# Optimization experiments

Measured on AMD Instinct MI355X. Metric: run time of the kernel, lower is better.

Reference implementation:

```python
import jax, jax.numpy as jnp
import numpy as np

D_MODEL = 1024
N_HEADS = 16
D_K = D_MODEL // N_HEADS
ROPE_BASE = 10000.0


def _rope_tables(seq_len, dim, dtype=jnp.float32):
    # standard rotary: inv_freq over even dims, angles broadcast over positions
    inv_freq = 1.0 / (ROPE_BASE ** (jnp.arange(0, dim, 2, dtype=jnp.float32) / dim))
    t = jnp.arange(seq_len, dtype=jnp.float32)
    freqs = jnp.outer(t, inv_freq)                  # [S, dim/2]
    emb = jnp.concatenate([freqs, freqs], axis=-1)   # [S, dim]
    return jnp.cos(emb).astype(dtype), jnp.sin(emb).astype(dtype)


def _rotate_half(x):
    x1, x2 = jnp.split(x, 2, axis=-1)
    return jnp.concatenate([-x2, x1], axis=-1)


def _apply_rope(x, cos, sin):
    # x: [B, H, S, d_k]; cos/sin: [S, d_k]
    return x * cos[None, None, :, :] + _rotate_half(x) * sin[None, None, :, :]


def setup_inputs() -> dict:
    key = jax.random.key(0)
    k1, k2, k3 = jax.random.split(key, 3)
    x = jax.random.normal(k1, (2, 2048, D_MODEL), dtype=jnp.float32)
    # torch Linear weights are [out, in]; store pre-transposed for x @ W
    scale = 1.0 / np.sqrt(D_MODEL)
    W_qkv = jax.random.normal(k2, (D_MODEL, 3 * D_MODEL), dtype=jnp.float32) * scale
    W_o = jax.random.normal(k3, (D_MODEL, D_MODEL), dtype=jnp.float32) * scale
    return {"x": x, "W_qkv": W_qkv, "W_o": W_o}


def reference(x, W_qkv, W_o):
    B, S, D = x.shape
    # fused QKV projection, then split into heads: [3, B, H, S, d_k]
    qkv = (x @ W_qkv).reshape(B, S, 3, N_HEADS, D_K).transpose(2, 0, 3, 1, 4)
    q, k, v = qkv[0], qkv[1], qkv[2]
    cos, sin = _rope_tables(S, D_K, x.dtype)
    q = _apply_rope(q, cos, sin)
    k = _apply_rope(k, cos, sin)
    # causal scaled dot-product attention (eval: dropout_p = 0)
    scores = jnp.einsum("bhqd,bhkd->bhqk", q, k) / jnp.sqrt(jnp.asarray(D_K, x.dtype))
    causal = jnp.tril(jnp.ones((S, S), dtype=bool))
    scores = jnp.where(causal[None, None], scores, jnp.asarray(-jnp.inf, x.dtype))
    attn = jax.nn.softmax(scores, axis=-1)
    out = jnp.einsum("bhqk,bhkd->bhqd", attn, v)          # [B, H, S, d_k]
    out = out.transpose(0, 2, 1, 3).reshape(B, S, D)       # [B, S, D]
    return out @ W_o
```

## Files before the change

### kernel.cpp

```cpp
#include <hip/hip_runtime.h>
#include <math.h>

#define B_ 2
#define S_ 2048
#define D_ 1024
#define H_ 16
#define DK_ 64
#define M_ (B_ * S_)
#define N3_ (3 * D_)

typedef __bf16 bf16;
typedef bf16 bf16x4 __attribute__((ext_vector_type(4)));
typedef bf16 bf16x8 __attribute__((ext_vector_type(8)));
typedef float f32x4 __attribute__((ext_vector_type(4)));
typedef short shortx4 __attribute__((ext_vector_type(4)));

#define GLL16(g, l)                                                     \
  __builtin_amdgcn_global_load_lds(                                     \
      (const __attribute__((address_space(1))) void*)(g),               \
      (__attribute__((address_space(3))) void*)(l), 16, 0, 0)


__global__ __launch_bounds__(256) void prep_k(
    const float* __restrict__ x, const float* __restrict__ Wqkv,
    const float* __restrict__ Wo, bf16* __restrict__ xb,
    bf16* __restrict__ Wqkv_bt, bf16* __restrict__ Wo_bt) {
  const int bx = blockIdx.x;
  if (bx < 4096) {
    int i = bx * 256 + threadIdx.x;
    float4 v = ((const float4*)x)[i];
    bf16x4 o = {(bf16)v.x, (bf16)v.y, (bf16)v.z, (bf16)v.w};
    ((bf16x4*)xb)[i] = o;
    return;
  }
  __shared__ float t[32][33];
  const float* src;
  bf16* dst;
  int R, C, cx, cy;
  if (bx < 4096 + 3072) {
    int b2 = bx - 4096;
    src = Wqkv; dst = Wqkv_bt; R = D_; C = N3_;
    cx = b2 % 96; cy = b2 / 96;
  } else {
    int b2 = bx - 7168;
    src = Wo; dst = Wo_bt; R = D_; C = D_;
    cx = b2 & 31; cy = b2 >> 5;
  }
  int r0 = cy * 32, c0 = cx * 32;
  int tx = threadIdx.x & 31, ty = threadIdx.x >> 5;
#pragma unroll
  for (int rr = 0; rr < 32; rr += 8)
    t[ty + rr][tx] = src[(size_t)(r0 + ty + rr) * C + c0 + tx];
  __syncthreads();
#pragma unroll
  for (int rr = 0; rr < 32; rr += 8)
    dst[(size_t)(c0 + ty + rr) * R + r0 + tx] = (bf16)t[tx][ty + rr];
}

#define GEMM_KLOOP(A, Bt, KDIM)                                              \
  __shared__ bf16 As[128 * 32];                                              \
  __shared__ bf16 Bs[128 * 32];                                              \
  const int tid = threadIdx.x;                                               \
  const int wave = tid >> 6, lane = tid & 63;                                \
  const int l15 = lane & 15, quad = lane >> 4;                               \
  const int wr = wave >> 1, wc = wave & 1;                                   \
  const int row0 = blockIdx.y * 128, col0 = blockIdx.x * 128;                \
  const int srow = (wave * 128 + lane) >> 2;                      \
  const int skc8 = (lane & 3) * 8;                                           \
  f32x4 acc[4][4] = {};                                                      \
  for (int k0 = 0; k0 < KDIM; k0 += 32) {                                    \
    __syncthreads();                                                         \
    _Pragma("unroll") for (int j = 0; j < 2; ++j) {                          \
      GLL16(A + (size_t)(row0 + srow + j * 16) * KDIM + k0 + skc8,           \
            &As[(wave * 128 + j * 64) * 8]);                                 \
      GLL16(Bt + (size_t)(col0 + srow + j * 16) * KDIM + k0 + skc8,          \
            &Bs[(wave * 128 + j * 64) * 8]);                                 \
    }                                                                        \
    __syncthreads();                                                         \
    bf16x8 af[4], bfr[4];                                                    \
    _Pragma("unroll") for (int i = 0; i < 4; ++i)                            \
        af[i] = *(const bf16x8*)&As[(wr * 64 + i * 16 + l15) * 32 + quad * 8]; \
    _Pragma("unroll") for (int t = 0; t < 4; ++t)                            \
        bfr[t] = *(const bf16x8*)&Bs[(wc * 64 + t * 16 + l15) * 32 + quad * 8]; \
    _Pragma("unroll") for (int i = 0; i < 4; ++i)                            \
        _Pragma("unroll") for (int t = 0; t < 4; ++t)                        \
            acc[i][t] = __builtin_amdgcn_mfma_f32_16x16x32_bf16(             \
                af[i], bfr[t], acc[i][t], 0, 0, 0);                          \
  }

__global__ __launch_bounds__(256) void gemm_qkv_mfma(
    const bf16* __restrict__ A, const bf16* __restrict__ Bt,
    bf16* __restrict__ Qb, bf16* __restrict__ Kb, bf16* __restrict__ VTb) {
  __shared__ bf16 Ct[4][32 * 72];
  GEMM_KLOOP(A, Bt, 1024)

  const int nb = col0 + wc * 64;
  const int which = nb >> 10;
  const int h = (nb >> 6) & 15;
  const float qsc = (which == 0) ? 0.125f : 1.0f;
  float freq[2];
#pragma unroll
  for (int t = 0; t < 2; ++t)
    freq[t] = exp2f((float)(t * 16 + l15) * -0.4152410118609203f);

  bf16* W = Ct[wave];
  const int mbase0 = row0 + wr * 64;
  const int bb = mbase0 >> 11;

#pragma unroll
  for (int ih = 0; ih < 2; ++ih) {
    __syncthreads();
    if (which == 2) {
#pragma unroll
      for (int i2 = 0; i2 < 2; ++i2) {
        int i = ih * 2 + i2;
#pragma unroll
        for (int r = 0; r < 4; ++r) {
          int sl = i2 * 16 + quad * 4 + r;
#pragma unroll
          for (int t = 0; t < 4; ++t)
            W[(t * 16 + l15) * 36 + sl] = (bf16)acc[i][t][r];
        }
      }
    } else {
#pragma unroll
      for (int i2 = 0; i2 < 2; ++i2) {
        int i = ih * 2 + i2;
#pragma unroll
        for (int r = 0; r < 4; ++r) {
          int ml = i2 * 16 + quad * 4 + r;
          int s = (mbase0 + i * 16 + quad * 4 + r) & (S_ - 1);
#pragma unroll
          for (int t = 0; t < 2; ++t) {
            float theta = (float)s * freq[t];
            float sn = __sinf(theta), cs = __cosf(theta);
            float x1 = acc[i][t][r], x2 = acc[i][t + 2][r];
            W[ml * 72 + t * 16 + l15] = (bf16)((x1 * cs - x2 * sn) * qsc);
            W[ml * 72 + t * 16 + l15 + 32] = (bf16)((x2 * cs + x1 * sn) * qsc);
          }
        }
      }
    }
    __syncthreads();
    const int s0 = (mbase0 + ih * 32) & (S_ - 1);
    if (which == 2) {
      bf16* vbase = VTb + ((size_t)(bb * H_ + h) * DK_) * (size_t)S_ + s0;
#pragma unroll
      for (int rr = 0; rr < 8; ++rr) {
        int d = rr * 8 + (lane >> 3);
        int c4 = (lane & 7) * 4;
        bf16x4 v = *(const bf16x4*)&W[d * 36 + c4];
        *(bf16x4*)(vbase + (size_t)d * S_ + c4) = v;
      }
    } else {
      bf16* basep = ((which == 0) ? Qb : Kb) +
                    (((size_t)(bb * H_ + h) * S_) + s0) * DK_;
#pragma unroll
      for (int rr = 0; rr < 4; ++rr) {
        int row = rr * 8 + (lane >> 3);
        int c8 = (lane & 7) * 8;
        bf16x8 v = *(const bf16x8*)&W[row * 72 + c8];
        *(bf16x8*)(basep + (size_t)row * DK_ + c8) = v;
      }
    }
  }
}

__global__ __launch_bounds__(256) void gemm_oproj_mfma(
    const bf16* __restrict__ A, const bf16* __restrict__ Bt,
    float* __restrict__ C) {
  GEMM_KLOOP(A, Bt, 1024)
#pragma unroll
  for (int i = 0; i < 4; ++i) {
#pragma unroll
    for (int r = 0; r < 4; ++r) {
      int m = row0 + wr * 64 + i * 16 + quad * 4 + r;
      float* dst = C + (size_t)m * D_ + col0 + wc * 64;
#pragma unroll
      for (int t = 0; t < 4; ++t) dst[t * 16 + l15] = acc[i][t][r];
    }
  }
}

__global__ __launch_bounds__(256) void attn_mfma(const bf16* __restrict__ Qb,
                                                 const bf16* __restrict__ Kb,
                                                 const bf16* __restrict__ VT,
                                                 bf16* __restrict__ Out) {
  __shared__ bf16 Ks[64 * 72];
  __shared__ bf16 Vs[64 * 68];

  const int tid = threadIdx.x;
  const int wave = tid >> 6, lane = tid & 63;
  const int l15 = lane & 15, quad = lane >> 4;

  const int bh = blockIdx.x & 31;
  const int q0 = (31 - (blockIdx.x >> 5)) * 64;
  const int qw = q0 + wave * 16;
  const size_t bh_off = (size_t)bh * (S_ * DK_);

  const bf16* qp = Qb + bh_off + (size_t)(qw + l15) * DK_ + quad * 8;
  bf16x8 qf0 = *(const bf16x8*)qp;
  bf16x8 qf1 = *(const bf16x8*)(qp + 32);

  f32x4 o_acc[4] = {};
  float lsum = 0.0f;

  for (int k0 = 0; k0 <= q0; k0 += 64) {
    __syncthreads();
#pragma unroll
    for (int it = 0; it < 2; ++it) {
      int e = tid + it * 256;
      int row = e >> 3, c8 = (e & 7) * 8;
      *(bf16x8*)&Ks[row * 72 + c8] =
          *(const bf16x8*)(Kb + bh_off + (size_t)(k0 + row) * DK_ + c8);
      *(bf16x8*)&Vs[row * 68 + c8] =
          *(const bf16x8*)(VT + bh_off + (size_t)row * S_ + k0 + c8);
    }
    __syncthreads();

    const bool dm = (k0 + 64 > qw);

    f32x4 st[4] = {};
#pragma unroll
    for (int t = 0; t < 4; ++t) {
      const bf16* kr = &Ks[(t * 16 + l15) * 72 + quad * 8];
      bf16x8 kf0 = *(const bf16x8*)kr;
      bf16x8 kf1 = *(const bf16x8*)(kr + 32);
      st[t] = __builtin_amdgcn_mfma_f32_16x16x32_bf16(kf0, qf0, st[t], 0, 0, 0);
      st[t] = __builtin_amdgcn_mfma_f32_16x16x32_bf16(kf1, qf1, st[t], 0, 0, 0);
    }

    bf16x4 pT[4];
    const int q = qw + l15;
#pragma unroll
    for (int t = 0; t < 4; ++t) {
#pragma unroll
      for (int r = 0; r < 4; ++r) {
        int key = k0 + t * 16 + quad * 4 + r;
        float p = __expf(st[t][r]);
        if (dm) p = (key <= q) ? p : 0.0f;
        lsum += p;
        pT[t][r] = (bf16)p;
      }
    }

#pragma unroll
    for (int u = 0; u < 4; ++u) {
#pragma unroll
      for (int t = 0; t < 4; ++t) {
        bf16x4 vf = *(const bf16x4*)&Vs[(u * 16 + l15) * 68 + t * 16 + quad * 4];
        o_acc[u] = __builtin_amdgcn_mfma_f32_16x16x16bf16_1k(
            __builtin_bit_cast(shortx4, pT[t]),
            __builtin_bit_cast(shortx4, vf), o_acc[u], 0, 0, 0);
      }
    }
  }

  const int b = bh >> 4, h = bh & 15;
  float l = lsum;
  l += __shfl_xor(l, 16, 64);
  l += __shfl_xor(l, 32, 64);
#pragma unroll
  for (int r = 0; r < 4; ++r) {
    float inv = 1.0f / __shfl(l, quad * 4 + r, 64);
    int q = qw + quad * 4 + r;
    bf16* op = Out + ((size_t)(b * S_ + q)) * D_ + h * DK_;
#pragma unroll
    for (int u = 0; u < 4; ++u)
      op[u * 16 + l15] = (bf16)(o_acc[u][r] * inv);
  }
}

extern "C" void kernel_launch(void* const* d_in, const int* in_sizes, int n_in,
                              void* d_out, int out_size, void* d_ws,
                              size_t ws_size, hipStream_t stream) {
  const float* x = (const float*)d_in[0];
  const float* Wqkv = (const float*)d_in[1];
  const float* Wo = (const float*)d_in[2];
  float* out = (float*)d_out;

  char* ws = (char*)d_ws;
  bf16* xb = (bf16*)(ws + 0);
  bf16* Wqkv_bt = (bf16*)(ws + (8u << 20));
  bf16* Wo_bt = (bf16*)(ws + (14u << 20));
  bf16* Qb = (bf16*)(ws + (16u << 20));
  bf16* Kb = (bf16*)(ws + (24u << 20));
  bf16* VTb = (bf16*)(ws + (32u << 20));
  bf16* AOb = (bf16*)(ws + (40u << 20));

  prep_k<<<4096 + 3072 + 1024, 256, 0, stream>>>(x, Wqkv, Wo, xb, Wqkv_bt,
                                                 Wo_bt);

  gemm_qkv_mfma<<<dim3(N3_ / 128, M_ / 128), 256, 0, stream>>>(xb, Wqkv_bt, Qb,
                                                               Kb, VTb);

  attn_mfma<<<B_ * H_ * (S_ / 64), 256, 0, stream>>>(Qb, Kb, VTb, AOb);

  gemm_oproj_mfma<<<dim3(D_ / 128, M_ / 128), 256, 0, stream>>>(AOb, Wo_bt, out);
}
```

Before: 176.9 us.

## Double-buffer attention K/V tiles, use exp2 with folded scale, retile O-projection

The attention kernel now double-buffers K and V tiles in shared memory. The next tile is loaded into registers while the current one is computed, which removes one barrier per iteration and hides global load latency. The softmax exponent switches to the hardware exp2, with log2(e) folded into the Q scale applied in the QKV epilogue. The output projection moves to 64x128 tiles to double the number of blocks for better CU occupancy, at the cost of less operand reuse per block.

```diff
diff --git a/kernel.cpp b/kernel.cpp
--- a/kernel.cpp
+++ b/kernel.cpp
@@ -19,6 +19,8 @@
   __builtin_amdgcn_global_load_lds(                                     \
       (const __attribute__((address_space(1))) void*)(g),               \
       (__attribute__((address_space(3))) void*)(l), 16, 0, 0)
+
+#define QSCALE 0.1803368801111204f
 
 
 __global__ __launch_bounds__(256) void prep_k(
@@ -97,7 +99,7 @@
   const int nb = col0 + wc * 64;
   const int which = nb >> 10;
   const int h = (nb >> 6) & 15;
-  const float qsc = (which == 0) ? 0.125f : 1.0f;
+  const float qsc = (which == 0) ? QSCALE : 1.0f;
   float freq[2];
 #pragma unroll
   for (int t = 0; t < 2; ++t)
@@ -169,15 +171,47 @@
 __global__ __launch_bounds__(256) void gemm_oproj_mfma(
     const bf16* __restrict__ A, const bf16* __restrict__ Bt,
     float* __restrict__ C) {
-  GEMM_KLOOP(A, Bt, 1024)
+  __shared__ bf16 As[64 * 32];
+  __shared__ bf16 Bs[128 * 32];
+  const int tid = threadIdx.x;
+  const int wave = tid >> 6, lane = tid & 63;
+  const int l15 = lane & 15, quad = lane >> 4;
+  const int row0 = blockIdx.y * 64, col0 = blockIdx.x * 128;
+  const int rA = tid >> 2, cA = (tid & 3) * 8;
+  f32x4 acc[4][2] = {};
+
+  for (int k0 = 0; k0 < 1024; k0 += 32) {
+    __syncthreads();
+    GLL16(A + (size_t)(row0 + rA) * 1024 + k0 + cA, &As[wave * 512]);
+#pragma unroll
+    for (int p = 0; p < 2; ++p) {
+      int e = tid + p * 256;
+      GLL16(Bt + (size_t)(col0 + (e >> 2)) * 1024 + k0 + (e & 3) * 8,
+            &Bs[(p * 256 + wave * 64) * 8]);
+    }
+    __syncthreads();
+    bf16x8 af[4], bfr[2];
+#pragma unroll
+    for (int i = 0; i < 4; ++i)
+      af[i] = *(const bf16x8*)&As[(i * 16 + l15) * 32 + quad * 8];
+#pragma unroll
+    for (int t = 0; t < 2; ++t)
+      bfr[t] = *(const bf16x8*)&Bs[(wave * 32 + t * 16 + l15) * 32 + quad * 8];
+#pragma unroll
+    for (int i = 0; i < 4; ++i)
+#pragma unroll
+      for (int t = 0; t < 2; ++t)
+        acc[i][t] = __builtin_amdgcn_mfma_f32_16x16x32_bf16(af[i], bfr[t],
+                                                            acc[i][t], 0, 0, 0);
+  }
 #pragma unroll
   for (int i = 0; i < 4; ++i) {
 #pragma unroll
     for (int r = 0; r < 4; ++r) {
-      int m = row0 + wr * 64 + i * 16 + quad * 4 + r;
-      float* dst = C + (size_t)m * D_ + col0 + wc * 64;
-#pragma unroll
-      for (int t = 0; t < 4; ++t) dst[t * 16 + l15] = acc[i][t][r];
+      int m = row0 + i * 16 + quad * 4 + r;
+      float* dst = C + (size_t)m * D_ + col0 + wave * 32;
+#pragma unroll
+      for (int t = 0; t < 2; ++t) dst[t * 16 + l15] = acc[i][t][r];
     }
   }
 }
@@ -186,8 +220,8 @@
                                                  const bf16* __restrict__ Kb,
                                                  const bf16* __restrict__ VT,
                                                  bf16* __restrict__ Out) {
-  __shared__ bf16 Ks[64 * 72];
-  __shared__ bf16 Vs[64 * 68];
+  __shared__ bf16 Ks[2][64 * 72];
+  __shared__ bf16 Vs[2][64 * 68];
 
   const int tid = threadIdx.x;
   const int wave = tid >> 6, lane = tid & 63;
@@ -198,6 +232,8 @@
   const int qw = q0 + wave * 16;
   const size_t bh_off = (size_t)bh * (S_ * DK_);
 
+  const int rowS = tid >> 3, c8S = (tid & 7) * 8;
+
   const bf16* qp = Qb + bh_off + (size_t)(qw + l15) * DK_ + quad * 8;
   bf16x8 qf0 = *(const bf16x8*)qp;
   bf16x8 qf1 = *(const bf16x8*)(qp + 32);
@@ -205,25 +241,45 @@
   f32x4 o_acc[4] = {};
   float lsum = 0.0f;
 
-  for (int k0 = 0; k0 <= q0; k0 += 64) {
-    __syncthreads();
-#pragma unroll
-    for (int it = 0; it < 2; ++it) {
-      int e = tid + it * 256;
-      int row = e >> 3, c8 = (e & 7) * 8;
-      *(bf16x8*)&Ks[row * 72 + c8] =
-          *(const bf16x8*)(Kb + bh_off + (size_t)(k0 + row) * DK_ + c8);
-      *(bf16x8*)&Vs[row * 68 + c8] =
-          *(const bf16x8*)(VT + bh_off + (size_t)row * S_ + k0 + c8);
-    }
-    __syncthreads();
-
+  bf16x8 kreg[2], vreg[2];
+#pragma unroll
+  for (int it = 0; it < 2; ++it) {
+    int row = rowS + it * 32;
+    kreg[it] = *(const bf16x8*)(Kb + bh_off + (size_t)row * DK_ + c8S);
+    vreg[it] = *(const bf16x8*)(VT + bh_off + (size_t)row * S_ + c8S);
+  }
+#pragma unroll
+  for (int it = 0; it < 2; ++it) {
+    int row = rowS + it * 32;
+    *(bf16x8*)&Ks[0][row * 72 + c8S] = kreg[it];
+    *(bf16x8*)&Vs[0][row * 68 + c8S] = vreg[it];
+  }
+  __syncthreads();
+
+  const int ntiles = (q0 >> 6) + 1;
+  for (int j = 0; j < ntiles; ++j) {
+    const int k0 = j * 64;
+    const int cur = j & 1;
+    const bool more = (j + 1 < ntiles);
+
+    if (more) {
+      int k1 = k0 + 64;
+#pragma unroll
+      for (int it = 0; it < 2; ++it) {
+        int row = rowS + it * 32;
+        kreg[it] = *(const bf16x8*)(Kb + bh_off + (size_t)(k1 + row) * DK_ + c8S);
+        vreg[it] = *(const bf16x8*)(VT + bh_off + (size_t)row * S_ + k1 + c8S);
+      }
+    }
+
+    const bf16* ksc = Ks[cur];
+    const bf16* vsc = Vs[cur];
     const bool dm = (k0 + 64 > qw);
 
     f32x4 st[4] = {};
 #pragma unroll
     for (int t = 0; t < 4; ++t) {
-      const bf16* kr = &Ks[(t * 16 + l15) * 72 + quad * 8];
+      const bf16* kr = &ksc[(t * 16 + l15) * 72 + quad * 8];
       bf16x8 kf0 = *(const bf16x8*)kr;
       bf16x8 kf1 = *(const bf16x8*)(kr + 32);
       st[t] = __builtin_amdgcn_mfma_f32_16x16x32_bf16(kf0, qf0, st[t], 0, 0, 0);
@@ -237,7 +293,7 @@
 #pragma unroll
       for (int r = 0; r < 4; ++r) {
         int key = k0 + t * 16 + quad * 4 + r;
-        float p = __expf(st[t][r]);
+        float p = __builtin_amdgcn_exp2f(st[t][r]);
         if (dm) p = (key <= q) ? p : 0.0f;
         lsum += p;
         pT[t][r] = (bf16)p;
@@ -248,11 +304,23 @@
     for (int u = 0; u < 4; ++u) {
 #pragma unroll
       for (int t = 0; t < 4; ++t) {
-        bf16x4 vf = *(const bf16x4*)&Vs[(u * 16 + l15) * 68 + t * 16 + quad * 4];
+        bf16x4 vf = *(const bf16x4*)&vsc[(u * 16 + l15) * 68 + t * 16 + quad * 4];
         o_acc[u] = __builtin_amdgcn_mfma_f32_16x16x16bf16_1k(
             __builtin_bit_cast(shortx4, pT[t]),
             __builtin_bit_cast(shortx4, vf), o_acc[u], 0, 0, 0);
       }
+    }
+
+    if (more) {
+      bf16* ksn = Ks[cur ^ 1];
+      bf16* vsn = Vs[cur ^ 1];
+#pragma unroll
+      for (int it = 0; it < 2; ++it) {
+        int row = rowS + it * 32;
+        *(bf16x8*)&ksn[row * 72 + c8S] = kreg[it];
+        *(bf16x8*)&vsn[row * 68 + c8S] = vreg[it];
+      }
+      __syncthreads();
     }
   }
 
@@ -296,5 +364,5 @@
 
   attn_mfma<<<B_ * H_ * (S_ / 64), 256, 0, stream>>>(Qb, Kb, VTb, AOb);
 
-  gemm_oproj_mfma<<<dim3(D_ / 128, M_ / 128), 256, 0, stream>>>(AOb, Wo_bt, out);
-}
+  gemm_oproj_mfma<<<dim3(D_ / 128, M_ / 64), 256, 0, stream>>>(AOb, Wo_bt, out);
+}
```

Result: slower. 181.5 us (+2.6%).
